# Performance work log

Hardware: AMD Instinct MI355X
Metric: run time of the kernel (lower is better)

## Reference

```python
import jax, jax.numpy as jnp
import numpy as np

B, S, D_MODEL, H, BLOCK = 2, 4096, 1024, 16, 512
HEAD = D_MODEL // H  # 64


def setup_inputs() -> dict:
    key = jax.random.key(0)
    ks = jax.random.split(key, 5)
    w_scale = 1.0 / np.sqrt(D_MODEL)  # variance_scaling(1.0,'fan_in','normal')-like magnitude
    return {
        "inputs_q": jax.random.normal(ks[0], (B, S, D_MODEL), jnp.float32),
        "Wq": jax.random.normal(ks[1], (D_MODEL, D_MODEL), jnp.float32) * w_scale,
        "bq": jnp.zeros((D_MODEL,), jnp.float32),
        "Wk": jax.random.normal(ks[2], (D_MODEL, D_MODEL), jnp.float32) * w_scale,
        "bk": jnp.zeros((D_MODEL,), jnp.float32),
        "Wv": jax.random.normal(ks[3], (D_MODEL, D_MODEL), jnp.float32) * w_scale,
        "bv": jnp.zeros((D_MODEL,), jnp.float32),
        "Wo": jax.random.normal(ks[4], (D_MODEL, D_MODEL), jnp.float32) * w_scale,
        "bo": jnp.zeros((D_MODEL,), jnp.float32),
    }


def _flash_attention(q, k, v):
    """Blocked online-softmax attention. q,k,v: [B,S,H,D] -> [B,S,H,D].

    Scans over KV blocks of size BLOCK, maintaining running max (m),
    running sum of exp (l), and unnormalized output (o), exactly matching
    the original module's blocked accumulation math (no mask/bias/dropout).
    """
    scale = 1.0 / jnp.sqrt(jnp.asarray(HEAD, q.dtype))
    n_kv_blocks = S // BLOCK
    # [n_blocks, B, BLOCK, H, D]
    kb = k.reshape(B, n_kv_blocks, BLOCK, H, HEAD).transpose(1, 0, 2, 3, 4)
    vb = v.reshape(B, n_kv_blocks, BLOCK, H, HEAD).transpose(1, 0, 2, 3, 4)

    o0 = jnp.zeros_like(q)                                   # [B,S,H,D]
    m0 = jnp.full((B, S, H), -jnp.inf, dtype=q.dtype)        # running max
    l0 = jnp.zeros((B, S, H), dtype=q.dtype)                 # running sum-exp

    def step(carry, kv):
        o, m, l = carry
        k_blk, v_blk = kv
        # [B,H,S,BLOCK] scores for all queries vs this kv block
        scores = jnp.einsum('bqhd,bkhd->bhqk', q, k_blk) * scale
        blk_max = jnp.max(scores, axis=-1).transpose(0, 2, 1)   # [B,S,H]
        new_m = jnp.maximum(m, blk_max)
        alpha = jnp.exp(m - new_m)                               # rescale old stats
        p = jnp.exp(scores - new_m.transpose(0, 2, 1)[..., None])
        new_l = alpha * l + jnp.sum(p, axis=-1).transpose(0, 2, 1)
        new_o = o * alpha[..., None] + jnp.einsum('bhqk,bkhd->bqhd', p, v_blk)
        return (new_o, new_m, new_l), None

    (o, m, l), _ = jax.lax.scan(step, (o0, m0, l0), (kb, vb))
    return o / l[..., None]


def reference(inputs_q, Wq, bq, Wk, bk, Wv, bv, Wo, bo):
    q = (inputs_q @ Wq + bq).reshape(B, S, H, HEAD)
    k = (inputs_q @ Wk + bk).reshape(B, S, H, HEAD)  # self-attention: k=v=q input
    v = (inputs_q @ Wv + bv).reshape(B, S, H, HEAD)
    x = _flash_attention(q, k, v).reshape(B, S, D_MODEL)
    return x @ Wo + bo
```

## Files before the change

### kernel.cpp

```cpp
#include <hip/hip_runtime.h>
#include <hip/hip_bf16.h>
#include <stdint.h>

#define B_ 2
#define S_ 4096
#define DM 1024
#define H_ 16
#define HD 64
#define M_TOT (B_*S_)

typedef unsigned short u16;
typedef short s16x8 __attribute__((ext_vector_type(8)));
typedef short s16x4 __attribute__((ext_vector_type(4)));
typedef float f32x4 __attribute__((ext_vector_type(4)));
typedef uint32_t u32x2 __attribute__((ext_vector_type(2)));

__device__ __forceinline__ u16 f2bf(float f){
  union { float fv; uint32_t u; } x; x.fv = f;
  uint32_t r = (x.u + 0x7fffu + ((x.u >> 16) & 1u)) >> 16;
  return (u16)r;
}

#if __has_builtin(__builtin_amdgcn_cvt_pk_bf16_f32)
typedef __bf16 bf16x2_t __attribute__((ext_vector_type(2)));
__device__ __forceinline__ uint32_t pkbf(float a, float b){
  union { bf16x2_t v; uint32_t u; } x;
  x.v = __builtin_amdgcn_cvt_pk_bf16_f32(a, b);
  return x.u;
}
#else
__device__ __forceinline__ uint32_t pkbf(float a, float b){
  union { float f; uint32_t u; } xa, xb; xa.f = a; xb.f = b;
  return __builtin_amdgcn_perm(xb.u + 0x8000u, xa.u + 0x8000u, 0x07060302u);
}
#endif

__device__ __forceinline__ void gld_lds16(const void* g, void* l){
  __builtin_amdgcn_global_load_lds((const __attribute__((address_space(1))) void*)g,
                                   (__attribute__((address_space(3))) void*)l, 16, 0, 0);
}

__global__ __launch_bounds__(256) void k_cvt_x(const float* __restrict__ x, u16* __restrict__ xb){
  size_t i = (size_t)blockIdx.x * 256 + threadIdx.x;
  const float4* p = (const float4*)x + i*2;
  float4 a = p[0], b = p[1];
  union { u16 u[8]; uint4 v; } o;
  o.u[0]=f2bf(a.x); o.u[1]=f2bf(a.y); o.u[2]=f2bf(a.z); o.u[3]=f2bf(a.w);
  o.u[4]=f2bf(b.x); o.u[5]=f2bf(b.y); o.u[6]=f2bf(b.z); o.u[7]=f2bf(b.w);
  ((uint4*)xb)[i] = o.v;
}

__global__ __launch_bounds__(256) void k_wt(const float* __restrict__ W0, const float* __restrict__ W1,
                                            const float* __restrict__ W2, const float* __restrict__ W3,
                                            u16* __restrict__ wt){
  const float* W = blockIdx.z==0?W0: blockIdx.z==1?W1: blockIdx.z==2?W2:W3;
  u16* out = wt + (size_t)blockIdx.z * DM * DM;
  int n0 = blockIdx.x*64, k0 = blockIdx.y*64;
  __shared__ u16 T[64*66];
  int t = threadIdx.x;
  #pragma unroll
  for (int i=0;i<4;i++){
    int idx = t + i*256;
    int kr = idx >> 4, n4 = idx & 15;
    float4 v = *(const float4*)(W + (size_t)(k0+kr)*DM + n0 + n4*4);
    T[(n4*4+0)*66 + kr] = f2bf(v.x);
    T[(n4*4+1)*66 + kr] = f2bf(v.y);
    T[(n4*4+2)*66 + kr] = f2bf(v.z);
    T[(n4*4+3)*66 + kr] = f2bf(v.w);
  }
  __syncthreads();
  #pragma unroll
  for (int i=0;i<2;i++){
    int idx = t + i*256;
    int n = idx >> 3, k8 = idx & 7;
    union { u16 u[8]; uint4 v; } o;
    #pragma unroll
    for (int j=0;j<8;j++) o.u[j] = T[n*66 + k8*8 + j];
    *(uint4*)(out + (size_t)(n0+n)*DM + k0 + k8*8) = o.v;
  }
}

__device__ __forceinline__ void gemm128(const u16* __restrict__ A, const u16* __restrict__ BT,
                                        const float* __restrict__ bias, bool brow, float scale,
                                        u16* __restrict__ outb, float* __restrict__ outf,
                                        int m0, int n0, int ldo){
  __shared__ __align__(16) u16 S[16384];
  u16* As = S;
  u16* Bs = S + 8192;
  int t = threadIdx.x;
  int lane = t & 63, w = t >> 6;
  int wm = w & 1, wn = w >> 1;
  int c16 = lane & 15, quad = lane >> 4;
  f32x4 acc[4][4] = {};
  const u16* ap[4]; const u16* bp[4];
  #pragma unroll
  for (int i=0;i<4;i++){
    int c = t + i*256;
    int row = c >> 3, scol = (c & 7) ^ (row & 7);
    ap[i] = A  + (size_t)(m0+row)*DM + scol*8;
    bp[i] = BT + (size_t)(n0+row)*DM + scol*8;
  }
  for (int k0 = 0; k0 < DM; k0 += 64){
    #pragma unroll
    for (int i=0;i<4;i++){
      int c = t + i*256;
      gld_lds16(ap[i] + k0, &As[c*8]);
      gld_lds16(bp[i] + k0, &Bs[c*8]);
    }
    __syncthreads();
    #pragma unroll
    for (int ks=0; ks<2; ks++){
      s16x8 af[4], bfr[4];
      #pragma unroll
      for (int mi=0;mi<4;mi++){
        int row = wm*64 + mi*16 + c16;
        af[mi] = *(const s16x8*)&As[row*64 + (((ks*4 + quad) ^ (row & 7))*8)];
      }
      #pragma unroll
      for (int ni=0;ni<4;ni++){
        int row = wn*64 + ni*16 + c16;
        bfr[ni] = *(const s16x8*)&Bs[row*64 + (((ks*4 + quad) ^ (row & 7))*8)];
      }
      #pragma unroll
      for (int mi=0;mi<4;mi++)
        #pragma unroll
        for (int ni=0;ni<4;ni++)
          acc[mi][ni] = __builtin_amdgcn_mfma_f32_16x16x32_bf16(af[mi], bfr[ni], acc[mi][ni], 0, 0, 0);
    }
    __syncthreads();
  }
  if (outb){
    #pragma unroll
    for (int mi=0;mi<4;mi++){
      #pragma unroll
      for (int ni=0;ni<4;ni++){
        int lc = wn*64 + ni*16 + c16;
        float bc = brow ? 0.0f : bias[n0 + lc];
        int chunk = lc >> 3, off = lc & 7;
        #pragma unroll
        for (int r=0;r<4;r++){
          int lrow = wm*64 + mi*16 + quad*4 + r;
          float bb = brow ? bias[m0 + lrow] : bc;
          float v = (acc[mi][ni][r] + bb) * scale;
          S[lrow*128 + ((chunk ^ (lrow & 7))<<3) + off] = f2bf(v);
        }
      }
    }
    __syncthreads();
    #pragma unroll
    for (int i=0;i<4;i++){
      int row = (t >> 3) + i*32;
      #pragma unroll
      for (int j=0;j<2;j++){
        int ch = (t & 7) + j*8;
        uint4 vv = *(const uint4*)&S[row*128 + ((ch ^ (row & 7))<<3)];
        *(uint4*)(outb + (size_t)(m0+row)*ldo + n0 + ch*8) = vv;
      }
    }
  } else {
    #pragma unroll
    for (int mi=0;mi<4;mi++){
      #pragma unroll
      for (int ni=0;ni<4;ni++){
        int col = n0 + wn*64 + ni*16 + c16;
        float bc = bias[col];
        #pragma unroll
        for (int r=0;r<4;r++){
          int row = m0 + wm*64 + mi*16 + quad*4 + r;
          outf[(size_t)row*ldo + col] = (acc[mi][ni][r] + bc) * scale;
        }
      }
    }
  }
}

#define CL2 0.18033688011112042f

__device__ __forceinline__ void gemm_swz(int wg, int& m0, int& n0){
  int xcd = wg & 7, loc = wg >> 3;
  m0 = ((xcd << 3) + (loc >> 3)) * 128;
  n0 = (loc & 7) * 128;
}

__global__ __launch_bounds__(256) void k_gemm_qkv(const u16* __restrict__ xb, const u16* __restrict__ wt,
                                                  const float* __restrict__ b0, const float* __restrict__ b1,
                                                  const float* __restrict__ b2,
                                                  u16* __restrict__ q, u16* __restrict__ k, u16* __restrict__ vt){
  int z = blockIdx.z;
  int m0, n0;
  gemm_swz(blockIdx.x + (blockIdx.y << 3), m0, n0);
  const u16* Aarg; const u16* Barg; const float* bias; float scale; u16* out;
  int mm, nn, ldo; bool brow;
  if (z == 2){
    Aarg = wt + 2*(size_t)DM*DM; Barg = xb; bias = b2; brow = true;  scale = 1.0f;
    out = vt; mm = n0; nn = m0; ldo = M_TOT;
  } else {
    Aarg = xb; Barg = wt + (size_t)z*DM*DM; bias = z ? b1 : b0; brow = false;
    scale = z ? 1.0f : CL2; out = z ? k : q; mm = m0; nn = n0; ldo = DM;
  }
  gemm128(Aarg, Barg, bias, brow, scale, out, nullptr, mm, nn, ldo);
}

__global__ __launch_bounds__(256) void k_gemm_out(const u16* __restrict__ ab, const u16* __restrict__ wto,
                                                  const float* __restrict__ bias, float* __restrict__ out){
  int m0, n0;
  gemm_swz(blockIdx.x + (blockIdx.y << 3), m0, n0);
  gemm128(ab, wto, bias, false, 1.0f, nullptr, out, m0, n0, DM);
}

__global__ __launch_bounds__(512, 2) void k_attn(const u16* __restrict__ qg, const u16* __restrict__ kg,
                                                 const u16* __restrict__ vtg, u16* __restrict__ ao){
  __shared__ __align__(16) char smem[67584];
  float* Ob  = (float*)smem;
  u16*   ObT = (u16*)smem;
  float* Lb  = (float*)(smem + 65536);

  int t = threadIdx.x, lane = t & 63, w = t >> 6;
  int c16 = lane & 15, quad = lane >> 4;
  int qq = w & 3, kh = w >> 2;
  int wg = blockIdx.x + (blockIdx.y << 4) + (blockIdx.z << 8);
  int xcd = wg & 7, loc = wg >> 3;
  int nw = (xcd << 6) + loc;
  int q0 = (nw & 15) * 256;
  int hb = nw >> 4;
  int h = hb & 15, b = hb >> 4;
  size_t rowbase = (size_t)b * S_;
  const u16* vbase = vtg + ((size_t)h*64)*M_TOT + b*S_;

  int krow0 = t >> 3,         ksw0 = ((t & 7) ^ (krow0 & 7));
  int krow1 = (t + 512) >> 3, ksw1 = ((t & 7) ^ (krow1 & 7));
  const u16* kgp0 = kg + (rowbase + krow0)*DM + h*64 + ksw0*8;
  const u16* kgp1 = kg + (rowbase + krow1)*DM + h*64 + ksw1*8;
  int vrow0 = t >> 4,         vsw0 = ((t & 15) ^ (vrow0 & 15));
  int vrow1 = (t + 512) >> 4, vsw1 = ((t & 15) ^ (vrow1 & 15));
  const u16* vgp0 = vbase + (size_t)vrow0*M_TOT + vsw0*8;
  const u16* vgp1 = vbase + (size_t)vrow1*M_TOT + vsw1*8;
  char* kd0 = smem + t*16;
  char* kd1 = smem + t*16 + 8192;
  char* vd0 = smem + 16384 + t*16;
  char* vd1 = smem + 16384 + t*16 + 8192;

  auto stage = [&](int boff, int kv0){
    size_t ko = (size_t)kv0 * DM;
    gld_lds16(kgp0 + ko, kd0 + boff);
    gld_lds16(kgp1 + ko, kd1 + boff);
    gld_lds16(vgp0 + kv0, vd0 + boff);
    gld_lds16(vgp1 + kv0, vd1 + boff);
  };

  stage(0, 0);

  s16x8 qf[4][2];
  #pragma unroll
  for (int nt=0;nt<4;nt++)
    #pragma unroll
    for (int ks=0;ks<2;ks++)
      qf[nt][ks] = *(const s16x8*)(qg + (rowbase + q0 + qq*64 + nt*16 + c16)*DM + h*64 + ks*32 + quad*8);

  f32x4 oacc[4][4] = {};
  float lacc[4] = {0.f,0.f,0.f,0.f};

  auto compute = [&](int boff){
    const u16* Kt = (const u16*)(smem + boff);
    const u16* Vt = (const u16*)(smem + boff + 16384);

    f32x4 sc[4][4] = {};
    #pragma unroll
    for (int mt=0;mt<4;mt++){
      #pragma unroll
      for (int ks=0;ks<2;ks++){
        s16x8 kf = *(const s16x8*)&Kt[(kh*64 + mt*16 + c16)*64 + (((ks*4 + quad) ^ (c16 & 7)) * 8)];
        #pragma unroll
        for (int nt=0;nt<4;nt++)
          sc[mt][nt] = __builtin_amdgcn_mfma_f32_16x16x32_bf16(kf, qf[nt][ks], sc[mt][nt], 0,0,0);
      }
    }

    uint32_t pk[4][4][2];
    #pragma unroll
    for (int mt=0;mt<4;mt++){
      #pragma unroll
      for (int nt=0;nt<4;nt++){
        float p0 = __builtin_amdgcn_exp2f(sc[mt][nt][0]);
        float p1 = __builtin_amdgcn_exp2f(sc[mt][nt][1]);
        float p2 = __builtin_amdgcn_exp2f(sc[mt][nt][2]);
        float p3 = __builtin_amdgcn_exp2f(sc[mt][nt][3]);
        lacc[nt] += (p0 + p1) + (p2 + p3);
        pk[mt][nt][0] = pkbf(p0, p1);
        pk[mt][nt][1] = pkbf(p2, p3);
      }
    }

    #pragma unroll
    for (int mp=0;mp<2;mp++){
      int mtA = mp*2, mtB = mp*2+1;
      #pragma unroll
      for (int dt=0;dt<4;dt++){
        union { s16x4 h[2]; s16x8 v8; } vf;
        vf.h[0] = *(const s16x4*)&Vt[(dt*16 + c16)*128 + (((kh*8 + mtA*2 + (quad>>1)) ^ c16) * 8) + (quad & 1)*4];
        vf.h[1] = *(const s16x4*)&Vt[(dt*16 + c16)*128 + (((kh*8 + mtB*2 + (quad>>1)) ^ c16) * 8) + (quad & 1)*4];
        #pragma unroll
        for (int nt=0;nt<4;nt++){
          union { uint32_t u[4]; s16x8 v; } pp;
          pp.u[0] = pk[mtA][nt][0]; pp.u[1] = pk[mtA][nt][1];
          pp.u[2] = pk[mtB][nt][0]; pp.u[3] = pk[mtB][nt][1];
          oacc[dt][nt] = __builtin_amdgcn_mfma_f32_16x16x32_bf16(vf.v8, pp.v, oacc[dt][nt], 0,0,0);
        }
      }
    }
  };

  #define NT (S_/128)
  #pragma unroll 1
  for (int kvt = 0; kvt < NT-1; ++kvt){
    stage(((kvt+1) & 1) * 32768, (kvt+1)*128);
    asm volatile("s_waitcnt vmcnt(4)" ::: "memory");
    __builtin_amdgcn_s_barrier();
    __builtin_amdgcn_sched_barrier(0);
    compute((kvt & 1) * 32768);
    __builtin_amdgcn_s_barrier();
    __builtin_amdgcn_sched_barrier(0);
  }
  asm volatile("s_waitcnt vmcnt(0)" ::: "memory");
  __builtin_amdgcn_s_barrier();
  __builtin_amdgcn_sched_barrier(0);
  compute(((NT-1) & 1) * 32768);

  float lw[4];
  #pragma unroll
  for (int nt=0;nt<4;nt++){
    float l = lacc[nt];
    l += __shfl_xor(l, 16);
    l += __shfl_xor(l, 32);
    lw[nt] = l;
  }
  __syncthreads();
  if (quad == 0){
    #pragma unroll
    for (int nt=0;nt<4;nt++) Lb[kh*256 + qq*64 + nt*16 + c16] = lw[nt];
  }
  uint32_t pko[4][4][2];
  float invl[4];
  #pragma unroll
  for (int dh=0; dh<2; dh++){
    if (kh == 1){
      #pragma unroll
      for (int dt2=0;dt2<2;dt2++)
        #pragma unroll
        for (int nt=0;nt<4;nt++)
          *(f32x4*)&Ob[(qq*64 + nt*16 + c16)*36 + dt2*16 + quad*4] = oacc[dh*2+dt2][nt];
    }
    __syncthreads();
    if (kh == 0){
      if (dh == 0){
        #pragma unroll
        for (int nt=0;nt<4;nt++){
          int ql = qq*64 + nt*16 + c16;
          invl[nt] = 1.0f / (Lb[ql] + Lb[256 + ql]);
        }
      }
      #pragma unroll
      for (int dt2=0;dt2<2;dt2++)
        #pragma unroll
        for (int nt=0;nt<4;nt++){
          f32x4 p = *(const f32x4*)&Ob[(qq*64 + nt*16 + c16)*36 + dt2*16 + quad*4];
          f32x4 o = oacc[dh*2+dt2][nt] + p;
          pko[dh*2+dt2][nt][0] = pkbf(o[0]*invl[nt], o[1]*invl[nt]);
          pko[dh*2+dt2][nt][1] = pkbf(o[2]*invl[nt], o[3]*invl[nt]);
        }
    }
    __syncthreads();
  }
  if (kh == 0){
    #pragma unroll
    for (int dt=0;dt<4;dt++)
      #pragma unroll
      for (int nt=0;nt<4;nt++){
        u32x2 pr; pr.x = pko[dt][nt][0]; pr.y = pko[dt][nt][1];
        *(u32x2*)&ObT[(qq*64 + nt*16 + c16)*72 + dt*16 + quad*4] = pr;
      }
  }
  __syncthreads();
  #pragma unroll
  for (int i=0;i<4;i++){
    int idx = t + i*512;
    int qr = idx >> 3, qc = (idx & 7)*8;
    *(s16x8*)(ao + (rowbase + q0 + qr)*DM + h*64 + qc) = *(const s16x8*)&ObT[qr*72 + qc];
  }
}

extern "C" void kernel_launch(void* const* d_in, const int* in_sizes, int n_in,
                              void* d_out, int out_size, void* d_ws, size_t ws_size,
                              hipStream_t stream){
  const float* x  = (const float*)d_in[0];
  const float* Wq = (const float*)d_in[1];
  const float* bq = (const float*)d_in[2];
  const float* Wk = (const float*)d_in[3];
  const float* bk = (const float*)d_in[4];
  const float* Wv = (const float*)d_in[5];
  const float* bv = (const float*)d_in[6];
  const float* Wo = (const float*)d_in[7];
  const float* bo = (const float*)d_in[8];

  char* ws = (char*)d_ws;
  const size_t XB = (size_t)M_TOT*DM*2;
  const size_t WTB = (size_t)4*DM*DM*2;
  u16* xb  = (u16*)(ws);
  u16* wt  = (u16*)(ws + XB);
  u16* qb  = (u16*)(ws + XB + WTB);
  u16* kb  = (u16*)(ws + XB + WTB + XB);
  u16* vtb = (u16*)(ws + XB + WTB + 2*XB);
  u16* aob = (u16*)(ws + XB + WTB + 3*XB);

  k_cvt_x<<<dim3((M_TOT*DM)/(256*8)), 256, 0, stream>>>(x, xb);
  k_wt<<<dim3(16,16,4), 256, 0, stream>>>(Wq, Wk, Wv, Wo, wt);
  k_gemm_qkv<<<dim3(8, M_TOT/128, 3), 256, 0, stream>>>(xb, wt, bq, bk, bv, qb, kb, vtb);
  k_attn<<<dim3(S_/256, H_, B_), 512, 0, stream>>>(qb, kb, vtb, aob);
  k_gemm_out<<<dim3(8, M_TOT/128), 256, 0, stream>>>(aob, wt + (size_t)3*DM*DM, bo, (float*)d_out);
}
```

Measured before the change: 346.3 us.

## Load K fragments directly into registers in attention, shrink LDS, merge prep kernels

```diff
diff --git a/kernel.cpp b/kernel.cpp
--- a/kernel.cpp
+++ b/kernel.cpp
@@ -40,28 +40,31 @@
                                    (__attribute__((address_space(3))) void*)l, 16, 0, 0);
 }
 
-__global__ __launch_bounds__(256) void k_cvt_x(const float* __restrict__ x, u16* __restrict__ xb){
-  size_t i = (size_t)blockIdx.x * 256 + threadIdx.x;
-  const float4* p = (const float4*)x + i*2;
-  float4 a = p[0], b = p[1];
-  union { u16 u[8]; uint4 v; } o;
-  o.u[0]=f2bf(a.x); o.u[1]=f2bf(a.y); o.u[2]=f2bf(a.z); o.u[3]=f2bf(a.w);
-  o.u[4]=f2bf(b.x); o.u[5]=f2bf(b.y); o.u[6]=f2bf(b.z); o.u[7]=f2bf(b.w);
-  ((uint4*)xb)[i] = o.v;
-}
-
-__global__ __launch_bounds__(256) void k_wt(const float* __restrict__ W0, const float* __restrict__ W1,
-                                            const float* __restrict__ W2, const float* __restrict__ W3,
-                                            u16* __restrict__ wt){
-  const float* W = blockIdx.z==0?W0: blockIdx.z==1?W1: blockIdx.z==2?W2:W3;
-  u16* out = wt + (size_t)blockIdx.z * DM * DM;
-  int n0 = blockIdx.x*64, k0 = blockIdx.y*64;
+__global__ __launch_bounds__(256) void k_prep(const float* __restrict__ x, u16* __restrict__ xb,
+                                              const float* __restrict__ W0, const float* __restrict__ W1,
+                                              const float* __restrict__ W2, const float* __restrict__ W3,
+                                              u16* __restrict__ wt){
   __shared__ u16 T[64*66];
   int t = threadIdx.x;
+  if (blockIdx.x < 4096){
+    size_t i = (size_t)blockIdx.x * 256 + t;
+    const float4* p = (const float4*)x + i*2;
+    float4 a = p[0], b = p[1];
+    union { u16 u[8]; uint4 v; } o;
+    o.u[0]=f2bf(a.x); o.u[1]=f2bf(a.y); o.u[2]=f2bf(a.z); o.u[3]=f2bf(a.w);
+    o.u[4]=f2bf(b.x); o.u[5]=f2bf(b.y); o.u[6]=f2bf(b.z); o.u[7]=f2bf(b.w);
+    ((uint4*)xb)[i] = o.v;
+    return;
+  }
+  int idx = blockIdx.x - 4096;
+  int bx = idx & 15, by = (idx >> 4) & 15, bz = idx >> 8;
+  const float* W = bz==0?W0: bz==1?W1: bz==2?W2:W3;
+  u16* out = wt + (size_t)bz * DM * DM;
+  int n0 = bx*64, k0 = by*64;
   #pragma unroll
   for (int i=0;i<4;i++){
-    int idx = t + i*256;
-    int kr = idx >> 4, n4 = idx & 15;
+    int id2 = t + i*256;
+    int kr = id2 >> 4, n4 = id2 & 15;
     float4 v = *(const float4*)(W + (size_t)(k0+kr)*DM + n0 + n4*4);
     T[(n4*4+0)*66 + kr] = f2bf(v.x);
     T[(n4*4+1)*66 + kr] = f2bf(v.y);
@@ -71,8 +74,8 @@
   __syncthreads();
   #pragma unroll
   for (int i=0;i<2;i++){
-    int idx = t + i*256;
-    int n = idx >> 3, k8 = idx & 7;
+    int id2 = t + i*256;
+    int n = id2 >> 3, k8 = id2 & 7;
     union { u16 u[8]; uint4 v; } o;
     #pragma unroll
     for (int j=0;j<8;j++) o.u[j] = T[n*66 + k8*8 + j];
@@ -208,12 +211,12 @@
   gemm128(ab, wto, bias, false, 1.0f, nullptr, out, m0, n0, DM);
 }
 
-__global__ __launch_bounds__(512, 2) void k_attn(const u16* __restrict__ qg, const u16* __restrict__ kg,
+__global__ __launch_bounds__(512, 4) void k_attn(const u16* __restrict__ qg, const u16* __restrict__ kg,
                                                  const u16* __restrict__ vtg, u16* __restrict__ ao){
-  __shared__ __align__(16) char smem[67584];
+  __shared__ __align__(16) char smem[38912];
   float* Ob  = (float*)smem;
   u16*   ObT = (u16*)smem;
-  float* Lb  = (float*)(smem + 65536);
+  float* Lb  = (float*)(smem + 36864);
 
   int t = threadIdx.x, lane = t & 63, w = t >> 6;
   int c16 = lane & 15, quad = lane >> 4;
@@ -227,27 +230,27 @@
   size_t rowbase = (size_t)b * S_;
   const u16* vbase = vtg + ((size_t)h*64)*M_TOT + b*S_;
 
-  int krow0 = t >> 3,         ksw0 = ((t & 7) ^ (krow0 & 7));
-  int krow1 = (t + 512) >> 3, ksw1 = ((t & 7) ^ (krow1 & 7));
-  const u16* kgp0 = kg + (rowbase + krow0)*DM + h*64 + ksw0*8;
-  const u16* kgp1 = kg + (rowbase + krow1)*DM + h*64 + ksw1*8;
   int vrow0 = t >> 4,         vsw0 = ((t & 15) ^ (vrow0 & 15));
   int vrow1 = (t + 512) >> 4, vsw1 = ((t & 15) ^ (vrow1 & 15));
   const u16* vgp0 = vbase + (size_t)vrow0*M_TOT + vsw0*8;
   const u16* vgp1 = vbase + (size_t)vrow1*M_TOT + vsw1*8;
-  char* kd0 = smem + t*16;
-  char* kd1 = smem + t*16 + 8192;
-  char* vd0 = smem + 16384 + t*16;
-  char* vd1 = smem + 16384 + t*16 + 8192;
+  char* vd0 = smem + t*16;
+  char* vd1 = smem + t*16 + 8192;
 
   auto stage = [&](int boff, int kv0){
-    size_t ko = (size_t)kv0 * DM;
-    gld_lds16(kgp0 + ko, kd0 + boff);
-    gld_lds16(kgp1 + ko, kd1 + boff);
     gld_lds16(vgp0 + kv0, vd0 + boff);
     gld_lds16(vgp1 + kv0, vd1 + boff);
   };
 
+  const u16* kgr = kg + (rowbase + kh*64 + c16)*DM + h*64 + quad*8;
+
+  s16x8 kf[4][2];
+  #pragma unroll
+  for (int mt=0;mt<4;mt++)
+    #pragma unroll
+    for (int ks=0;ks<2;ks++)
+      kf[mt][ks] = *(const s16x8*)(kgr + (size_t)(mt*16)*DM + ks*32);
+
   stage(0, 0);
 
   s16x8 qf[4][2];
@@ -260,20 +263,26 @@
   f32x4 oacc[4][4] = {};
   float lacc[4] = {0.f,0.f,0.f,0.f};
 
-  auto compute = [&](int boff){
-    const u16* Kt = (const u16*)(smem + boff);
-    const u16* Vt = (const u16*)(smem + boff + 16384);
+  auto compute = [&](int boff, int kvn, bool pref){
+    const u16* Vt = (const u16*)(smem + boff);
 
     f32x4 sc[4][4] = {};
     #pragma unroll
     for (int mt=0;mt<4;mt++){
       #pragma unroll
       for (int ks=0;ks<2;ks++){
-        s16x8 kf = *(const s16x8*)&Kt[(kh*64 + mt*16 + c16)*64 + (((ks*4 + quad) ^ (c16 & 7)) * 8)];
         #pragma unroll
         for (int nt=0;nt<4;nt++)
-          sc[mt][nt] = __builtin_amdgcn_mfma_f32_16x16x32_bf16(kf, qf[nt][ks], sc[mt][nt], 0,0,0);
-      }
+          sc[mt][nt] = __builtin_amdgcn_mfma_f32_16x16x32_bf16(kf[mt][ks], qf[nt][ks], sc[mt][nt], 0,0,0);
+      }
+    }
+
+    if (pref){
+      #pragma unroll
+      for (int mt=0;mt<4;mt++)
+        #pragma unroll
+        for (int ks=0;ks<2;ks++)
+          kf[mt][ks] = *(const s16x8*)(kgr + (size_t)(kvn + mt*16)*DM + ks*32);
     }
 
     uint32_t pk[4][4][2];
@@ -310,21 +319,23 @@
     }
   };
 
+  __builtin_amdgcn_sched_barrier(0);
+
   #define NT (S_/128)
   #pragma unroll 1
-  for (int kvt = 0; kvt < NT-1; ++kvt){
-    stage(((kvt+1) & 1) * 32768, (kvt+1)*128);
-    asm volatile("s_waitcnt vmcnt(4)" ::: "memory");
+  for (int kvt = 0; kvt < NT; ++kvt){
+    if (kvt+1 < NT){
+      stage(((kvt+1) & 1) * 16384, (kvt+1)*128);
+      asm volatile("s_waitcnt vmcnt(2)" ::: "memory");
+    } else {
+      asm volatile("s_waitcnt vmcnt(0)" ::: "memory");
+    }
     __builtin_amdgcn_s_barrier();
     __builtin_amdgcn_sched_barrier(0);
-    compute((kvt & 1) * 32768);
+    compute((kvt & 1) * 16384, (kvt+1)*128, kvt+1 < NT);
     __builtin_amdgcn_s_barrier();
     __builtin_amdgcn_sched_barrier(0);
   }
-  asm volatile("s_waitcnt vmcnt(0)" ::: "memory");
-  __builtin_amdgcn_s_barrier();
-  __builtin_amdgcn_sched_barrier(0);
-  compute(((NT-1) & 1) * 32768);
 
   float lw[4];
   #pragma unroll
@@ -412,8 +423,7 @@
   u16* vtb = (u16*)(ws + XB + WTB + 2*XB);
   u16* aob = (u16*)(ws + XB + WTB + 3*XB);
 
-  k_cvt_x<<<dim3((M_TOT*DM)/(256*8)), 256, 0, stream>>>(x, xb);
-  k_wt<<<dim3(16,16,4), 256, 0, stream>>>(Wq, Wk, Wv, Wo, wt);
+  k_prep<<<dim3(4096 + 1024), 256, 0, stream>>>(x, xb, Wq, Wk, Wv, Wo, wt);
   k_gemm_qkv<<<dim3(8, M_TOT/128, 3), 256, 0, stream>>>(xb, wt, bq, bk, bv, qb, kb, vtb);
   k_attn<<<dim3(S_/256, H_, B_), 512, 0, stream>>>(qb, kb, vtb, aob);
   k_gemm_out<<<dim3(8, M_TOT/128), 256, 0, stream>>>(aob, wt + (size_t)3*DM*DM, bo, (float*)d_out);
```

New measurement: 1.189 ms. +243.4%, slower.

## Enlarge GEMM tiles to 256x128 with 512 threads and merge prep kernels

Applied to the files above, without the earlier changes.

```diff
diff --git a/kernel.cpp b/kernel.cpp
--- a/kernel.cpp
+++ b/kernel.cpp
@@ -40,28 +40,31 @@
                                    (__attribute__((address_space(3))) void*)l, 16, 0, 0);
 }
 
-__global__ __launch_bounds__(256) void k_cvt_x(const float* __restrict__ x, u16* __restrict__ xb){
-  size_t i = (size_t)blockIdx.x * 256 + threadIdx.x;
-  const float4* p = (const float4*)x + i*2;
-  float4 a = p[0], b = p[1];
-  union { u16 u[8]; uint4 v; } o;
-  o.u[0]=f2bf(a.x); o.u[1]=f2bf(a.y); o.u[2]=f2bf(a.z); o.u[3]=f2bf(a.w);
-  o.u[4]=f2bf(b.x); o.u[5]=f2bf(b.y); o.u[6]=f2bf(b.z); o.u[7]=f2bf(b.w);
-  ((uint4*)xb)[i] = o.v;
-}
-
-__global__ __launch_bounds__(256) void k_wt(const float* __restrict__ W0, const float* __restrict__ W1,
-                                            const float* __restrict__ W2, const float* __restrict__ W3,
-                                            u16* __restrict__ wt){
-  const float* W = blockIdx.z==0?W0: blockIdx.z==1?W1: blockIdx.z==2?W2:W3;
-  u16* out = wt + (size_t)blockIdx.z * DM * DM;
-  int n0 = blockIdx.x*64, k0 = blockIdx.y*64;
+__global__ __launch_bounds__(256) void k_prep(const float* __restrict__ x, u16* __restrict__ xb,
+                                              const float* __restrict__ W0, const float* __restrict__ W1,
+                                              const float* __restrict__ W2, const float* __restrict__ W3,
+                                              u16* __restrict__ wt){
   __shared__ u16 T[64*66];
   int t = threadIdx.x;
+  if (blockIdx.x < 4096){
+    size_t i = (size_t)blockIdx.x * 256 + t;
+    const float4* p = (const float4*)x + i*2;
+    float4 a = p[0], b = p[1];
+    union { u16 u[8]; uint4 v; } o;
+    o.u[0]=f2bf(a.x); o.u[1]=f2bf(a.y); o.u[2]=f2bf(a.z); o.u[3]=f2bf(a.w);
+    o.u[4]=f2bf(b.x); o.u[5]=f2bf(b.y); o.u[6]=f2bf(b.z); o.u[7]=f2bf(b.w);
+    ((uint4*)xb)[i] = o.v;
+    return;
+  }
+  int idx = blockIdx.x - 4096;
+  int bx = idx & 15, by = (idx >> 4) & 15, bz = idx >> 8;
+  const float* W = bz==0?W0: bz==1?W1: bz==2?W2:W3;
+  u16* out = wt + (size_t)bz * DM * DM;
+  int n0 = bx*64, k0 = by*64;
   #pragma unroll
   for (int i=0;i<4;i++){
-    int idx = t + i*256;
-    int kr = idx >> 4, n4 = idx & 15;
+    int id2 = t + i*256;
+    int kr = id2 >> 4, n4 = id2 & 15;
     float4 v = *(const float4*)(W + (size_t)(k0+kr)*DM + n0 + n4*4);
     T[(n4*4+0)*66 + kr] = f2bf(v.x);
     T[(n4*4+1)*66 + kr] = f2bf(v.y);
@@ -71,8 +74,8 @@
   __syncthreads();
   #pragma unroll
   for (int i=0;i<2;i++){
-    int idx = t + i*256;
-    int n = idx >> 3, k8 = idx & 7;
+    int id2 = t + i*256;
+    int n = id2 >> 3, k8 = id2 & 7;
     union { u16 u[8]; uint4 v; } o;
     #pragma unroll
     for (int j=0;j<8;j++) o.u[j] = T[n*66 + k8*8 + j];
@@ -80,45 +83,48 @@
   }
 }
 
-__device__ __forceinline__ void gemm128(const u16* __restrict__ A, const u16* __restrict__ BT,
+__device__ __forceinline__ void gemm256(const u16* __restrict__ A, const u16* __restrict__ BT,
                                         const float* __restrict__ bias, bool brow, float scale,
                                         u16* __restrict__ outb, float* __restrict__ outf,
                                         int m0, int n0, int ldo){
-  __shared__ __align__(16) u16 S[16384];
+  __shared__ __align__(16) u16 S[24576];
   u16* As = S;
-  u16* Bs = S + 8192;
+  u16* Bs = S + 16384;
   int t = threadIdx.x;
   int lane = t & 63, w = t >> 6;
-  int wm = w & 1, wn = w >> 1;
+  int wr = w >> 1, wc = w & 1;
   int c16 = lane & 15, quad = lane >> 4;
   f32x4 acc[4][4] = {};
-  const u16* ap[4]; const u16* bp[4];
+  const u16* ap[4]; const u16* bp[2];
   #pragma unroll
   for (int i=0;i<4;i++){
-    int c = t + i*256;
+    int c = t + i*512;
     int row = c >> 3, scol = (c & 7) ^ (row & 7);
-    ap[i] = A  + (size_t)(m0+row)*DM + scol*8;
+    ap[i] = A + (size_t)(m0+row)*DM + scol*8;
+  }
+  #pragma unroll
+  for (int i=0;i<2;i++){
+    int c = t + i*512;
+    int row = c >> 3, scol = (c & 7) ^ (row & 7);
     bp[i] = BT + (size_t)(n0+row)*DM + scol*8;
   }
   for (int k0 = 0; k0 < DM; k0 += 64){
     #pragma unroll
-    for (int i=0;i<4;i++){
-      int c = t + i*256;
-      gld_lds16(ap[i] + k0, &As[c*8]);
-      gld_lds16(bp[i] + k0, &Bs[c*8]);
-    }
+    for (int i=0;i<4;i++) gld_lds16(ap[i] + k0, &As[(t + i*512)*8]);
+    #pragma unroll
+    for (int i=0;i<2;i++) gld_lds16(bp[i] + k0, &Bs[(t + i*512)*8]);
     __syncthreads();
     #pragma unroll
     for (int ks=0; ks<2; ks++){
       s16x8 af[4], bfr[4];
       #pragma unroll
       for (int mi=0;mi<4;mi++){
-        int row = wm*64 + mi*16 + c16;
+        int row = wr*64 + mi*16 + c16;
         af[mi] = *(const s16x8*)&As[row*64 + (((ks*4 + quad) ^ (row & 7))*8)];
       }
       #pragma unroll
       for (int ni=0;ni<4;ni++){
-        int row = wn*64 + ni*16 + c16;
+        int row = wc*64 + ni*16 + c16;
         bfr[ni] = *(const s16x8*)&Bs[row*64 + (((ks*4 + quad) ^ (row & 7))*8)];
       }
       #pragma unroll
@@ -131,42 +137,45 @@
   }
   if (outb){
     #pragma unroll
+    for (int hh=0; hh<2; hh++){
+      if ((wr >> 1) == hh){
+        #pragma unroll
+        for (int mi=0;mi<4;mi++){
+          #pragma unroll
+          for (int ni=0;ni<4;ni++){
+            int lc = wc*64 + ni*16 + c16;
+            float bc = brow ? 0.0f : bias[n0 + lc];
+            int chunk = lc >> 3, off = lc & 7;
+            #pragma unroll
+            for (int r=0;r<4;r++){
+              int lrow = (wr & 1)*64 + mi*16 + quad*4 + r;
+              float bb = brow ? bias[m0 + hh*128 + lrow] : bc;
+              float v = (acc[mi][ni][r] + bb) * scale;
+              S[lrow*128 + ((chunk ^ (lrow & 7))<<3) + off] = f2bf(v);
+            }
+          }
+        }
+      }
+      __syncthreads();
+      #pragma unroll
+      for (int i=0;i<4;i++){
+        int c = t + i*512;
+        int row = c >> 4, ch = c & 15;
+        uint4 vv = *(const uint4*)&S[row*128 + ((ch ^ (row & 7))<<3) + 0];
+        *(uint4*)(outb + (size_t)(m0 + hh*128 + row)*ldo + n0 + ch*8) = vv;
+      }
+      __syncthreads();
+    }
+  } else {
+    #pragma unroll
     for (int mi=0;mi<4;mi++){
       #pragma unroll
       for (int ni=0;ni<4;ni++){
-        int lc = wn*64 + ni*16 + c16;
-        float bc = brow ? 0.0f : bias[n0 + lc];
-        int chunk = lc >> 3, off = lc & 7;
+        int col = n0 + wc*64 + ni*16 + c16;
+        float bc = bias[col];
         #pragma unroll
         for (int r=0;r<4;r++){
-          int lrow = wm*64 + mi*16 + quad*4 + r;
-          float bb = brow ? bias[m0 + lrow] : bc;
-          float v = (acc[mi][ni][r] + bb) * scale;
-          S[lrow*128 + ((chunk ^ (lrow & 7))<<3) + off] = f2bf(v);
-        }
-      }
-    }
-    __syncthreads();
-    #pragma unroll
-    for (int i=0;i<4;i++){
-      int row = (t >> 3) + i*32;
-      #pragma unroll
-      for (int j=0;j<2;j++){
-        int ch = (t & 7) + j*8;
-        uint4 vv = *(const uint4*)&S[row*128 + ((ch ^ (row & 7))<<3)];
-        *(uint4*)(outb + (size_t)(m0+row)*ldo + n0 + ch*8) = vv;
-      }
-    }
-  } else {
-    #pragma unroll
-    for (int mi=0;mi<4;mi++){
-      #pragma unroll
-      for (int ni=0;ni<4;ni++){
-        int col = n0 + wn*64 + ni*16 + c16;
-        float bc = bias[col];
-        #pragma unroll
-        for (int r=0;r<4;r++){
-          int row = m0 + wm*64 + mi*16 + quad*4 + r;
+          int row = m0 + wr*64 + mi*16 + quad*4 + r;
           outf[(size_t)row*ldo + col] = (acc[mi][ni][r] + bc) * scale;
         }
       }
@@ -176,36 +185,34 @@
 
 #define CL2 0.18033688011112042f
 
-__device__ __forceinline__ void gemm_swz(int wg, int& m0, int& n0){
+__device__ __forceinline__ void gemm_swz256(int wg, int& mt, int& nt){
   int xcd = wg & 7, loc = wg >> 3;
-  m0 = ((xcd << 3) + (loc >> 3)) * 128;
-  n0 = (loc & 7) * 128;
-}
-
-__global__ __launch_bounds__(256) void k_gemm_qkv(const u16* __restrict__ xb, const u16* __restrict__ wt,
+  mt = (xcd << 2) + (loc >> 3);
+  nt = loc & 7;
+}
+
+__global__ __launch_bounds__(512) void k_gemm_qkv(const u16* __restrict__ xb, const u16* __restrict__ wt,
                                                   const float* __restrict__ b0, const float* __restrict__ b1,
                                                   const float* __restrict__ b2,
                                                   u16* __restrict__ q, u16* __restrict__ k, u16* __restrict__ vt){
   int z = blockIdx.z;
-  int m0, n0;
-  gemm_swz(blockIdx.x + (blockIdx.y << 3), m0, n0);
-  const u16* Aarg; const u16* Barg; const float* bias; float scale; u16* out;
-  int mm, nn, ldo; bool brow;
+  int mt, nt;
+  gemm_swz256(blockIdx.x + (blockIdx.y << 3), mt, nt);
   if (z == 2){
-    Aarg = wt + 2*(size_t)DM*DM; Barg = xb; bias = b2; brow = true;  scale = 1.0f;
-    out = vt; mm = n0; nn = m0; ldo = M_TOT;
+    int mV = (nt >> 1), nV = mt*2 + (nt & 1);
+    gemm256(wt + 2*(size_t)DM*DM, xb, b2, true, 1.0f, vt, nullptr,
+            mV*256, nV*128, M_TOT);
   } else {
-    Aarg = xb; Barg = wt + (size_t)z*DM*DM; bias = z ? b1 : b0; brow = false;
-    scale = z ? 1.0f : CL2; out = z ? k : q; mm = m0; nn = n0; ldo = DM;
-  }
-  gemm128(Aarg, Barg, bias, brow, scale, out, nullptr, mm, nn, ldo);
-}
-
-__global__ __launch_bounds__(256) void k_gemm_out(const u16* __restrict__ ab, const u16* __restrict__ wto,
+    gemm256(xb, wt + (size_t)z*DM*DM, z ? b1 : b0, false, z ? 1.0f : CL2,
+            z ? k : q, nullptr, mt*256, nt*128, DM);
+  }
+}
+
+__global__ __launch_bounds__(512) void k_gemm_out(const u16* __restrict__ ab, const u16* __restrict__ wto,
                                                   const float* __restrict__ bias, float* __restrict__ out){
-  int m0, n0;
-  gemm_swz(blockIdx.x + (blockIdx.y << 3), m0, n0);
-  gemm128(ab, wto, bias, false, 1.0f, nullptr, out, m0, n0, DM);
+  int mt, nt;
+  gemm_swz256(blockIdx.x + (blockIdx.y << 3), mt, nt);
+  gemm256(ab, wto, bias, false, 1.0f, nullptr, out, mt*256, nt*128, DM);
 }
 
 __global__ __launch_bounds__(512, 2) void k_attn(const u16* __restrict__ qg, const u16* __restrict__ kg,
@@ -412,9 +419,8 @@
   u16* vtb = (u16*)(ws + XB + WTB + 2*XB);
   u16* aob = (u16*)(ws + XB + WTB + 3*XB);
 
-  k_cvt_x<<<dim3((M_TOT*DM)/(256*8)), 256, 0, stream>>>(x, xb);
-  k_wt<<<dim3(16,16,4), 256, 0, stream>>>(Wq, Wk, Wv, Wo, wt);
-  k_gemm_qkv<<<dim3(8, M_TOT/128, 3), 256, 0, stream>>>(xb, wt, bq, bk, bv, qb, kb, vtb);
+  k_prep<<<dim3(4096 + 1024), 256, 0, stream>>>(x, xb, Wq, Wk, Wv, Wo, wt);
+  k_gemm_qkv<<<dim3(8, 32, 3), 512, 0, stream>>>(xb, wt, bq, bk, bv, qb, kb, vtb);
   k_attn<<<dim3(S_/256, H_, B_), 512, 0, stream>>>(qb, kb, vtb, aob);
-  k_gemm_out<<<dim3(8, M_TOT/128), 256, 0, stream>>>(aob, wt + (size_t)3*DM*DM, bo, (float*)d_out);
-}
+  k_gemm_out<<<dim3(8, 32), 512, 0, stream>>>(aob, wt + (size_t)3*DM*DM, bo, (float*)d_out);
+}
```

After: 355.4 us. +2.6%, slower.
